# Performance work log

Measured on AMD Instinct MI355X. Metric: run time of the kernel, lower is better.

## Reference

```python
import jax, jax.numpy as jnp
import numpy as np

T, IN, HID, OUT, B = 256, 1024, 1024, 1024, 128


def setup_inputs() -> dict:
    key = jax.random.key(0)
    k1, k2, k3, k4 = jax.random.split(key, 4)
    return {
        "inputs": jax.random.normal(k1, (T, IN, B), dtype=jnp.float32),
        "h_prev": jnp.zeros((HID, B), dtype=jnp.float32),
        "Wxh": jax.random.normal(k2, (HID, IN), dtype=jnp.float32) * 0.01,
        "Whh": jax.random.normal(k3, (HID, HID), dtype=jnp.float32) * 0.01,
        "Why": jax.random.normal(k4, (OUT, HID), dtype=jnp.float32) * 0.01,
        "bh": jnp.zeros((HID, 1), dtype=jnp.float32),
        "by": jnp.zeros((OUT, 1), dtype=jnp.float32),
    }


def reference(inputs, h_prev, Wxh, Whh, Why, bh, by):
    # inputs: [T, IN, B]; h: [HID, B]
    def step(h, x):
        h = jnp.tanh(Wxh @ x + Whh @ h + bh)
        y = Why @ h + by
        return h, y

    h_final, ys = jax.lax.scan(step, h_prev, inputs)
    return ys, h_final  # ys: [T, OUT, B], h_final: [HID, B]
```

## Files before the change

kernel.cpp:

```cpp
#include <hip/hip_runtime.h>
#include <cmath>

#define T_STEPS 256
#define DIN  1024
#define DHID 1024
#define DOUT 1024
#define NB   128
#define BH   (DHID*NB)

typedef unsigned short u16;
typedef unsigned int   u32;
typedef unsigned long long u64;
typedef __attribute__((ext_vector_type(8))) __bf16 bf16x8;
typedef __attribute__((ext_vector_type(4))) float  f32x4;

__device__ __forceinline__ u16 f2bf(float f){
  u32 u = __builtin_bit_cast(u32, f);
  u32 r = (u + 0x7fffu + ((u >> 16) & 1u)) >> 16;
  return (u16)r;
}
__device__ __forceinline__ float bf2f(u16 h){
  u32 u = ((u32)h) << 16;
  return __builtin_bit_cast(float, u);
}

__device__ __forceinline__ u32 ld_agent_u32(const u32* p){
  return __hip_atomic_load(p, __ATOMIC_RELAXED, __HIP_MEMORY_SCOPE_AGENT);
}
__device__ __forceinline__ void st_agent_u64(u64* p, u64 v){
  __hip_atomic_store(p, v, __ATOMIC_RELAXED, __HIP_MEMORY_SCOPE_AGENT);
}
__device__ __forceinline__ void gload_lds16(const void* g, void* l){
  __builtin_amdgcn_global_load_lds(
      (const __attribute__((address_space(1))) unsigned int*)g,
      (__attribute__((address_space(3))) unsigned int*)l, 16, 0, 0);
}

__global__ __launch_bounds__(256) void wconv(const float* __restrict__ w0,
                                             const float* __restrict__ w1,
                                             const float* __restrict__ w2,
                                             u16* __restrict__ dst){
  const int idx = blockIdx.x*256 + threadIdx.x;
  const int seg = idx >> 18;
  const int off = idx & 262143;
  const float* src = seg==0 ? w0 : (seg==1 ? w1 : w2);
  const float4 v = ((const float4*)src)[off];
  ushort4 o = make_ushort4(f2bf(v.x), f2bf(v.y), f2bf(v.z), f2bf(v.w));
  ((ushort4*)dst)[idx] = o;
}

__global__ __launch_bounds__(256) void hprevT(const float* __restrict__ hp,
                                              u16* __restrict__ HT0){
  const int tid = blockIdx.x*256 + threadIdx.x;
  const int b = tid >> 10, m = tid & 1023;
  HT0[tid] = f2bf(hp[(size_t)m*NB + b]);
}

__global__ __launch_bounds__(256) void xT_k(const float* __restrict__ x,
                                            u16* __restrict__ xt){
  __shared__ float tile[64][65];
  const int t  = blockIdx.z;
  const int k0 = blockIdx.y*64;
  const int b0 = blockIdx.x*64;
  const int tx = threadIdx.x & 63, ty = threadIdx.x >> 6;
  const float* src = x + (size_t)t*DIN*NB + (size_t)k0*NB + b0;
#pragma unroll
  for(int r=0;r<16;r++){ int k = r*4 + ty; tile[k][tx] = src[(size_t)k*NB + tx]; }
  __syncthreads();
  u16* dst = xt + (size_t)t*NB*DIN + (size_t)b0*DIN + k0;
#pragma unroll
  for(int r=0;r<16;r++){ int b = r*4 + ty; dst[(size_t)b*DIN + tx] = f2bf(tile[tx][b]); }
}

__global__ __launch_bounds__(256) void gemm_xw(const u16* __restrict__ XT,
                                               const u16* __restrict__ WxB,
                                               const float* __restrict__ bh,
                                               u16* __restrict__ AT){
  const int t  = blockIdx.y;
  const int mj = blockIdx.x;
  __shared__ __align__(16) u16 As[128*40];
  __shared__ __align__(16) u16 Bs[128*40];
  const u16* aG = XT + (size_t)t*NB*DIN;
  const u16* bG = WxB + (size_t)mj*128*DIN;
  const int tid = threadIdx.x;
  const int lane = tid & 63, w = tid >> 6;
  const int wr = (w & 1)*64, wc = (w >> 1)*64;
  const int l15 = lane & 15, q = lane >> 4;
  const int sr = tid >> 2;
  const int sk = (tid & 3)*8;

  f32x4 acc[4][4] = {};
  uint4 pa0 = *(const uint4*)&aG[(size_t)sr*DIN + sk];
  uint4 pa1 = *(const uint4*)&aG[(size_t)(sr+64)*DIN + sk];
  uint4 pb0 = *(const uint4*)&bG[(size_t)sr*DIN + sk];
  uint4 pb1 = *(const uint4*)&bG[(size_t)(sr+64)*DIN + sk];

  for(int it = 0; it < DIN/32; ++it){
    __syncthreads();
    *(uint4*)&As[sr*40 + sk]      = pa0;
    *(uint4*)&As[(sr+64)*40 + sk] = pa1;
    *(uint4*)&Bs[sr*40 + sk]      = pb0;
    *(uint4*)&Bs[(sr+64)*40 + sk] = pb1;
    __syncthreads();
    if(it < DIN/32 - 1){
      const int k0 = (it+1)*32;
      pa0 = *(const uint4*)&aG[(size_t)sr*DIN + k0 + sk];
      pa1 = *(const uint4*)&aG[(size_t)(sr+64)*DIN + k0 + sk];
      pb0 = *(const uint4*)&bG[(size_t)sr*DIN + k0 + sk];
      pb1 = *(const uint4*)&bG[(size_t)(sr+64)*DIN + k0 + sk];
    }
    bf16x8 af[4], bf[4];
#pragma unroll
    for(int i=0;i<4;i++) af[i] = *(const bf16x8*)&As[(wr + i*16 + l15)*40 + q*8];
#pragma unroll
    for(int j=0;j<4;j++) bf[j] = *(const bf16x8*)&Bs[(wc + j*16 + l15)*40 + q*8];
#pragma unroll
    for(int i=0;i<4;i++)
#pragma unroll
      for(int j=0;j<4;j++)
        acc[i][j] = __builtin_amdgcn_mfma_f32_16x16x32_bf16(af[i], bf[j], acc[i][j], 0,0,0);
  }

  u16* out = AT + (size_t)t*NB*DHID;
#pragma unroll
  for(int j=0;j<4;j++){
    const int mg = mj*128 + wc + j*16 + l15;
    const float bhv = bh[mg];
#pragma unroll
    for(int i=0;i<4;i++){
#pragma unroll
      for(int r=0;r<4;r++){
        const int bg = wr + i*16 + q*4 + r;
        out[(size_t)bg*DHID + mg] = f2bf(acc[i][j][r] + bhv);
      }
    }
  }
}

#define RSTEP_BLOCKS 64
__global__ __launch_bounds__(256, 1) void rnn_steps(const u16* __restrict__ WhB,
                                                    const u16* __restrict__ AT,
                                                    u16* __restrict__ HT,
                                                    u32* __restrict__ flags){
  const int mslice = blockIdx.x & 7;
  const int bg     = blockIdx.x >> 3;
  __shared__ __align__(16) u16 Hs[16*1032];
  __shared__ __align__(16) u16 Es[4*16*40];
  const int tid = threadIdx.x;
  const int lane = tid & 63, w = tid >> 6;
  const int l15 = lane & 15, q = lane >> 4, q8 = q*8;
  const int mw = mslice*128 + w*32;

  bf16x8 wf0[32], wf1[32];
  { const u16* ws0 = WhB + (size_t)(mw + l15)*DHID;
    const u16* ws1 = WhB + (size_t)(mw + 16 + l15)*DHID;
#pragma unroll
    for(int i=0;i<32;i++){ wf0[i] = *(const bf16x8*)&ws0[i*32 + q8];
                           wf1[i] = *(const bf16x8*)&ws1[i*32 + q8]; }
  }

  const int eb = lane >> 2, ec = lane & 3;
  const u32* fl = &flags[(size_t)(bg*8 + (lane & 7))*32];

  u16 avn[2][4];
#pragma unroll
  for(int h=0;h<2;h++)
#pragma unroll
    for(int r=0;r<4;r++)
      avn[h][r] = AT[(size_t)(bg*16 + q*4 + r)*DHID + mw + h*16 + l15];

  for(int t=0; t<T_STEPS; ++t){
    while(ld_agent_u32(fl) < (u32)t)
      ;

    { const u16* hbase = HT + (size_t)t*BH + (size_t)(bg*16)*DHID;
#pragma unroll
      for(int i=0;i<4;i++){
        const int row = w*4 + i;
#pragma unroll
        for(int half=0; half<2; half++){
          const u16* gp = hbase + (size_t)row*DHID + half*512 + lane*8;
          gload_lds16(gp, &Hs[row*1032 + half*512]);
        }
      }
    }
    __syncthreads();

    f32x4 a0e = {0,0,0,0}, a0o = {0,0,0,0}, a1e = {0,0,0,0}, a1o = {0,0,0,0};
#pragma unroll
    for(int kk=0;kk<32;kk+=2){
      bf16x8 ae = *(const bf16x8*)&Hs[l15*1032 + kk*32 + q8];
      bf16x8 ao = *(const bf16x8*)&Hs[l15*1032 + (kk+1)*32 + q8];
      a0e = __builtin_amdgcn_mfma_f32_16x16x32_bf16(ae, wf0[kk],   a0e, 0,0,0);
      a1e = __builtin_amdgcn_mfma_f32_16x16x32_bf16(ae, wf1[kk],   a1e, 0,0,0);
      a0o = __builtin_amdgcn_mfma_f32_16x16x32_bf16(ao, wf0[kk+1], a0o, 0,0,0);
      a1o = __builtin_amdgcn_mfma_f32_16x16x32_bf16(ao, wf1[kk+1], a1o, 0,0,0);
    }
    f32x4 acc0 = a0e + a0o, acc1 = a1e + a1o;

    u16* Ew = Es + w*640;
#pragma unroll
    for(int r=0;r<4;r++){
      float v0 = acc0[r] + bf2f(avn[0][r]);
      float v1 = acc1[r] + bf2f(avn[1][r]);
      Ew[(q*4+r)*40 + l15]      = f2bf(tanhf(v0));
      Ew[(q*4+r)*40 + 16 + l15] = f2bf(tanhf(v1));
    }
    __threadfence_block();
    u64 h0 = *(const u64*)&Ew[eb*40 + ec*8];
    u64 h1 = *(const u64*)&Ew[eb*40 + ec*8 + 4];
    u64* Hn = (u64*)(HT + (size_t)(t+1)*BH + (size_t)(bg*16 + eb)*DHID + mw + ec*8);
    st_agent_u64(Hn,     h0);
    st_agent_u64(Hn + 1, h1);

    asm volatile("s_waitcnt vmcnt(0)" ::: "memory");
    __syncthreads();

    if(t < T_STEPS-1){
      if(tid == 0)
        __hip_atomic_store(&flags[(size_t)(bg*8 + mslice)*32], (u32)(t+1),
                           __ATOMIC_RELAXED, __HIP_MEMORY_SCOPE_AGENT);
      const u16* At = AT + (size_t)(t+1)*BH;
#pragma unroll
      for(int h=0;h<2;h++)
#pragma unroll
        for(int r=0;r<4;r++)
          avn[h][r] = At[(size_t)(bg*16 + q*4 + r)*DHID + mw + h*16 + l15];
    }
  }
}

__global__ __launch_bounds__(256) void gemm_hy(const u16* __restrict__ WyB,
                                               const u16* __restrict__ HT,
                                               const float* __restrict__ by,
                                               float* __restrict__ Y){
  const int t  = blockIdx.y;
  const int mi = blockIdx.x;
  __shared__ __align__(16) u16 As[128*40];
  __shared__ __align__(16) u16 Bs[128*40];
  const u16* aG = WyB + (size_t)mi*128*DHID;
  const u16* bG = HT  + (size_t)(t+1)*BH;
  const int tid = threadIdx.x;
  const int lane = tid & 63, w = tid >> 6;
  const int wr = (w & 1)*64, wc = (w >> 1)*64;
  const int l15 = lane & 15, q = lane >> 4;
  const int sr = tid >> 2;
  const int sk = (tid & 3)*8;

  f32x4 acc[4][4] = {};
  uint4 pa0 = *(const uint4*)&aG[(size_t)sr*DHID + sk];
  uint4 pa1 = *(const uint4*)&aG[(size_t)(sr+64)*DHID + sk];
  uint4 pb0 = *(const uint4*)&bG[(size_t)sr*DHID + sk];
  uint4 pb1 = *(const uint4*)&bG[(size_t)(sr+64)*DHID + sk];

  for(int it = 0; it < DHID/32; ++it){
    __syncthreads();
    *(uint4*)&As[sr*40 + sk]      = pa0;
    *(uint4*)&As[(sr+64)*40 + sk] = pa1;
    *(uint4*)&Bs[sr*40 + sk]      = pb0;
    *(uint4*)&Bs[(sr+64)*40 + sk] = pb1;
    __syncthreads();
    if(it < DHID/32 - 1){
      const int k0 = (it+1)*32;
      pa0 = *(const uint4*)&aG[(size_t)sr*DHID + k0 + sk];
      pa1 = *(const uint4*)&aG[(size_t)(sr+64)*DHID + k0 + sk];
      pb0 = *(const uint4*)&bG[(size_t)sr*DHID + k0 + sk];
      pb1 = *(const uint4*)&bG[(size_t)(sr+64)*DHID + k0 + sk];
    }
    bf16x8 af[4], bf[4];
#pragma unroll
    for(int i=0;i<4;i++) af[i] = *(const bf16x8*)&As[(wr + i*16 + l15)*40 + q*8];
#pragma unroll
    for(int j=0;j<4;j++) bf[j] = *(const bf16x8*)&Bs[(wc + j*16 + l15)*40 + q*8];
#pragma unroll
    for(int i=0;i<4;i++)
#pragma unroll
      for(int j=0;j<4;j++)
        acc[i][j] = __builtin_amdgcn_mfma_f32_16x16x32_bf16(af[i], bf[j], acc[i][j], 0,0,0);
  }

  float* out = Y + (size_t)t*DOUT*NB;
#pragma unroll
  for(int i=0;i<4;i++){
#pragma unroll
    for(int r=0;r<4;r++){
      const int og = mi*128 + wr + i*16 + q*4 + r;
      const float byv = by[og];
#pragma unroll
      for(int j=0;j<4;j++){
        const int bg = wc + j*16 + l15;
        out[(size_t)og*NB + bg] = acc[i][j][r] + byv;
      }
    }
  }
}

__global__ __launch_bounds__(256) void hfinal(const u16* __restrict__ HT,
                                              float* __restrict__ dst){
  const int tid = blockIdx.x*256 + threadIdx.x;
  const int m = tid >> 7, b = tid & 127;
  dst[tid] = bf2f(HT[(size_t)T_STEPS*BH + (size_t)b*DHID + m]);
}

extern "C" void kernel_launch(void* const* d_in, const int* in_sizes, int n_in,
                              void* d_out, int out_size, void* d_ws, size_t ws_size,
                              hipStream_t stream)
{
  const float* x   = (const float*)d_in[0];
  const float* hp  = (const float*)d_in[1];
  const float* wxh = (const float*)d_in[2];
  const float* whh = (const float*)d_in[3];
  const float* why = (const float*)d_in[4];
  const float* bh  = (const float*)d_in[5];
  const float* by  = (const float*)d_in[6];
  float* out = (float*)d_out;

  u16* WxB = (u16*)d_ws;
  u16* WhB = WxB + (size_t)1024*1024;
  u16* WyB = WhB + (size_t)1024*1024;
  u16* HT  = WyB + (size_t)1024*1024;
  u32* flags = (u32*)(HT + (size_t)(T_STEPS+1)*BH);

  u16* XT = (u16*)d_out;
  u16* AT = XT + (size_t)T_STEPS*NB*DIN;

  wconv  <<<3072, 256, 0, stream>>>(wxh, whh, why, WxB);
  hprevT <<<512,  256, 0, stream>>>(hp, HT);
  xT_k   <<<dim3(2,16,T_STEPS), 256, 0, stream>>>(x, XT);
  gemm_xw<<<dim3(8,T_STEPS),    256, 0, stream>>>(XT, WxB, bh, AT);
  (void)hipMemsetAsync(flags, 0, 8192, stream);
  rnn_steps<<<RSTEP_BLOCKS, 256, 0, stream>>>(WhB, AT, HT, flags);
  gemm_hy<<<dim3(8,T_STEPS), 256, 0, stream>>>(WyB, HT, by, out);
  hfinal <<<512, 256, 0, stream>>>(HT, out + (size_t)T_STEPS*DOUT*NB);
}
```

Before: 1.426 ms.

## Load recurrent h directly into registers, transpose input-projection layout, fast tanh

The recurrent step kernel now reads the previous hidden state straight from global memory into MFMA operand registers. This replaces the LDS staging and the block barrier that preceded each step's matmul. The input-projection GEMM swaps its operands so it writes a [HID, B] layout, which lets each lane fetch its four bias-plus-input values with one 64-bit load instead of eight scalar loads. It also skips polling its own slice's flag, and uses an exp-based tanh in place of tanhf. The risks are more VGPR pressure (32 extra bf16x8 registers per thread), memory visibility now relying on an empty asm barrier, and slightly different tanh accuracy.

```diff
diff --git a/kernel.cpp b/kernel.cpp
--- a/kernel.cpp
+++ b/kernel.cpp
@@ -23,17 +23,16 @@
   u32 u = ((u32)h) << 16;
   return __builtin_bit_cast(float, u);
 }
+__device__ __forceinline__ float tanh_fast(float x){
+  float e = __expf(2.0f*x);
+  return 1.0f - 2.0f/(e + 1.0f);
+}
 
 __device__ __forceinline__ u32 ld_agent_u32(const u32* p){
   return __hip_atomic_load(p, __ATOMIC_RELAXED, __HIP_MEMORY_SCOPE_AGENT);
 }
 __device__ __forceinline__ void st_agent_u64(u64* p, u64 v){
   __hip_atomic_store(p, v, __ATOMIC_RELAXED, __HIP_MEMORY_SCOPE_AGENT);
-}
-__device__ __forceinline__ void gload_lds16(const void* g, void* l){
-  __builtin_amdgcn_global_load_lds(
-      (const __attribute__((address_space(1))) unsigned int*)g,
-      (__attribute__((address_space(3))) unsigned int*)l, 16, 0, 0);
 }
 
 __global__ __launch_bounds__(256) void wconv(const float* __restrict__ w0,
@@ -75,13 +74,13 @@
 __global__ __launch_bounds__(256) void gemm_xw(const u16* __restrict__ XT,
                                                const u16* __restrict__ WxB,
                                                const float* __restrict__ bh,
-                                               u16* __restrict__ AT){
+                                               u16* __restrict__ ATm){
   const int t  = blockIdx.y;
   const int mj = blockIdx.x;
   __shared__ __align__(16) u16 As[128*40];
   __shared__ __align__(16) u16 Bs[128*40];
-  const u16* aG = XT + (size_t)t*NB*DIN;
-  const u16* bG = WxB + (size_t)mj*128*DIN;
+  const u16* aG = WxB + (size_t)mj*128*DIN;
+  const u16* bG = XT + (size_t)t*NB*DIN;
   const int tid = threadIdx.x;
   const int lane = tid & 63, w = tid >> 6;
   const int wr = (w & 1)*64, wc = (w >> 1)*64;
@@ -121,17 +120,17 @@
         acc[i][j] = __builtin_amdgcn_mfma_f32_16x16x32_bf16(af[i], bf[j], acc[i][j], 0,0,0);
   }
 
-  u16* out = AT + (size_t)t*NB*DHID;
-#pragma unroll
-  for(int j=0;j<4;j++){
-    const int mg = mj*128 + wc + j*16 + l15;
-    const float bhv = bh[mg];
-#pragma unroll
-    for(int i=0;i<4;i++){
-#pragma unroll
-      for(int r=0;r<4;r++){
-        const int bg = wr + i*16 + q*4 + r;
-        out[(size_t)bg*DHID + mg] = f2bf(acc[i][j][r] + bhv);
+  u16* out = ATm + (size_t)t*BH;
+#pragma unroll
+  for(int i=0;i<4;i++){
+#pragma unroll
+    for(int r=0;r<4;r++){
+      const int mg = mj*128 + wr + i*16 + q*4 + r;
+      const float bhv = bh[mg];
+#pragma unroll
+      for(int j=0;j<4;j++){
+        const int bl = wc + j*16 + l15;
+        out[(size_t)mg*NB + bl] = f2bf(acc[i][j][r] + bhv);
       }
     }
   }
@@ -139,12 +138,11 @@
 
 #define RSTEP_BLOCKS 64
 __global__ __launch_bounds__(256, 1) void rnn_steps(const u16* __restrict__ WhB,
-                                                    const u16* __restrict__ AT,
+                                                    const u16* __restrict__ ATm,
                                                     u16* __restrict__ HT,
                                                     u32* __restrict__ flags){
   const int mslice = blockIdx.x & 7;
   const int bg     = blockIdx.x >> 3;
-  __shared__ __align__(16) u16 Hs[16*1032];
   __shared__ __align__(16) u16 Es[4*16*40];
   const int tid = threadIdx.x;
   const int lane = tid & 63, w = tid >> 6;
@@ -161,50 +159,40 @@
 
   const int eb = lane >> 2, ec = lane & 3;
   const u32* fl = &flags[(size_t)(bg*8 + (lane & 7))*32];
-
-  u16 avn[2][4];
-#pragma unroll
-  for(int h=0;h<2;h++)
-#pragma unroll
-    for(int r=0;r<4;r++)
-      avn[h][r] = AT[(size_t)(bg*16 + q*4 + r)*DHID + mw + h*16 + l15];
+  const bool needfl = ((lane & 7) != mslice);
+
+  u64 av0 = *(const u64*)(ATm + (size_t)(mw + l15)*NB + bg*16 + q*4);
+  u64 av1 = *(const u64*)(ATm + (size_t)(mw + 16 + l15)*NB + bg*16 + q*4);
 
   for(int t=0; t<T_STEPS; ++t){
-    while(ld_agent_u32(fl) < (u32)t)
-      ;
-
-    { const u16* hbase = HT + (size_t)t*BH + (size_t)(bg*16)*DHID;
-#pragma unroll
-      for(int i=0;i<4;i++){
-        const int row = w*4 + i;
-#pragma unroll
-        for(int half=0; half<2; half++){
-          const u16* gp = hbase + (size_t)row*DHID + half*512 + lane*8;
-          gload_lds16(gp, &Hs[row*1032 + half*512]);
-        }
-      }
-    }
-    __syncthreads();
+    if(needfl){
+      while(ld_agent_u32(fl) < (u32)t)
+        ;
+    }
+    asm volatile("" ::: "memory");
+
+    const u16* hb = HT + (size_t)t*BH + (size_t)(bg*16 + l15)*DHID + q8;
+    bf16x8 af[32];
+#pragma unroll
+    for(int kk=0;kk<32;kk++) af[kk] = *(const bf16x8*)&hb[kk*32];
 
     f32x4 a0e = {0,0,0,0}, a0o = {0,0,0,0}, a1e = {0,0,0,0}, a1o = {0,0,0,0};
 #pragma unroll
     for(int kk=0;kk<32;kk+=2){
-      bf16x8 ae = *(const bf16x8*)&Hs[l15*1032 + kk*32 + q8];
-      bf16x8 ao = *(const bf16x8*)&Hs[l15*1032 + (kk+1)*32 + q8];
-      a0e = __builtin_amdgcn_mfma_f32_16x16x32_bf16(ae, wf0[kk],   a0e, 0,0,0);
-      a1e = __builtin_amdgcn_mfma_f32_16x16x32_bf16(ae, wf1[kk],   a1e, 0,0,0);
-      a0o = __builtin_amdgcn_mfma_f32_16x16x32_bf16(ao, wf0[kk+1], a0o, 0,0,0);
-      a1o = __builtin_amdgcn_mfma_f32_16x16x32_bf16(ao, wf1[kk+1], a1o, 0,0,0);
+      a0e = __builtin_amdgcn_mfma_f32_16x16x32_bf16(af[kk],   wf0[kk],   a0e, 0,0,0);
+      a1e = __builtin_amdgcn_mfma_f32_16x16x32_bf16(af[kk],   wf1[kk],   a1e, 0,0,0);
+      a0o = __builtin_amdgcn_mfma_f32_16x16x32_bf16(af[kk+1], wf0[kk+1], a0o, 0,0,0);
+      a1o = __builtin_amdgcn_mfma_f32_16x16x32_bf16(af[kk+1], wf1[kk+1], a1o, 0,0,0);
     }
     f32x4 acc0 = a0e + a0o, acc1 = a1e + a1o;
 
     u16* Ew = Es + w*640;
 #pragma unroll
     for(int r=0;r<4;r++){
-      float v0 = acc0[r] + bf2f(avn[0][r]);
-      float v1 = acc1[r] + bf2f(avn[1][r]);
-      Ew[(q*4+r)*40 + l15]      = f2bf(tanhf(v0));
-      Ew[(q*4+r)*40 + 16 + l15] = f2bf(tanhf(v1));
+      float v0 = acc0[r] + bf2f((u16)(av0 >> (16*r)));
+      float v1 = acc1[r] + bf2f((u16)(av1 >> (16*r)));
+      Ew[(q*4+r)*40 + l15]      = f2bf(tanh_fast(v0));
+      Ew[(q*4+r)*40 + 16 + l15] = f2bf(tanh_fast(v1));
     }
     __threadfence_block();
     u64 h0 = *(const u64*)&Ew[eb*40 + ec*8];
@@ -220,12 +208,9 @@
       if(tid == 0)
         __hip_atomic_store(&flags[(size_t)(bg*8 + mslice)*32], (u32)(t+1),
                            __ATOMIC_RELAXED, __HIP_MEMORY_SCOPE_AGENT);
-      const u16* At = AT + (size_t)(t+1)*BH;
-#pragma unroll
-      for(int h=0;h<2;h++)
-#pragma unroll
-        for(int r=0;r<4;r++)
-          avn[h][r] = At[(size_t)(bg*16 + q*4 + r)*DHID + mw + h*16 + l15];
+      const u16* At = ATm + (size_t)(t+1)*BH;
+      av0 = *(const u64*)(At + (size_t)(mw + l15)*NB + bg*16 + q*4);
+      av1 = *(const u64*)(At + (size_t)(mw + 16 + l15)*NB + bg*16 + q*4);
     }
   }
 }
@@ -321,15 +306,15 @@
   u16* HT  = WyB + (size_t)1024*1024;
   u32* flags = (u32*)(HT + (size_t)(T_STEPS+1)*BH);
 
-  u16* XT = (u16*)d_out;
-  u16* AT = XT + (size_t)T_STEPS*NB*DIN;
+  u16* XT  = (u16*)d_out;
+  u16* ATm = XT + (size_t)T_STEPS*NB*DIN;
 
   wconv  <<<3072, 256, 0, stream>>>(wxh, whh, why, WxB);
   hprevT <<<512,  256, 0, stream>>>(hp, HT);
   xT_k   <<<dim3(2,16,T_STEPS), 256, 0, stream>>>(x, XT);
-  gemm_xw<<<dim3(8,T_STEPS),    256, 0, stream>>>(XT, WxB, bh, AT);
+  gemm_xw<<<dim3(8,T_STEPS),    256, 0, stream>>>(XT, WxB, bh, ATm);
   (void)hipMemsetAsync(flags, 0, 8192, stream);
-  rnn_steps<<<RSTEP_BLOCKS, 256, 0, stream>>>(WhB, AT, HT, flags);
+  rnn_steps<<<RSTEP_BLOCKS, 256, 0, stream>>>(WhB, ATm, HT, flags);
   gemm_hy<<<dim3(8,T_STEPS), 256, 0, stream>>>(WyB, HT, by, out);
   hfinal <<<512, 256, 0, stream>>>(HT, out + (size_t)T_STEPS*DOUT*NB);
 }
```

Result: slower. 2.377 ms (+66.7%).
